# Kernel tuning notes

Hardware: AMD Instinct MI355X
Metric: run time of the kernel (lower is better)

The kernel has to match this reference:

```python
import jax, jax.numpy as jnp
import numpy as np

NUM_EXPERTS = 64
HIDDEN = 2048
SINKHORN_ITERS = 30
EPS = 1e-08


def setup_inputs() -> dict:
    key = jax.random.key(0)
    k1, k2 = jax.random.split(key)
    hidden_states = jax.random.normal(k1, (4, 2048, HIDDEN), dtype=jnp.float32)
    # torch Linear default init ~ U(-1/sqrt(H), 1/sqrt(H))
    bound = 1.0 / np.sqrt(HIDDEN)
    W = jax.random.uniform(k2, (NUM_EXPERTS, HIDDEN), dtype=jnp.float32,
                           minval=-bound, maxval=bound)
    return {"hidden_states": hidden_states, "W": W}


def _sinkhorn(cost, num_iters=SINKHORN_ITERS):
    # cost: (T, E) float32 logits
    cost = jnp.exp(cost)
    T, E = cost.shape
    d0 = jnp.ones((T,), dtype=cost.dtype)
    d1 = jnp.ones((E,), dtype=cost.dtype)

    def body(i, carry):
        d0, d1 = carry
        d0 = (1.0 / T) / (jnp.sum(d1 * cost, axis=1) + EPS)
        d1 = (1.0 / E) / (jnp.sum(d0[:, None] * cost, axis=0) + EPS)
        return (d0, d1)

    d0, d1 = jax.lax.fori_loop(0, num_iters, body, (d0, d1))
    return d1 * cost * d0[:, None]


def reference(hidden_states, W):
    # router logits: (B, S, H) @ (H, E) -> flatten to (T, E)
    logits = jnp.einsum('bsh,eh->bse', hidden_states, W)
    router_logits = logits.reshape(-1, NUM_EXPERTS)
    # expert affinities (original uses float64 sigmoid; use float32 for jax default)
    expert_affinities = jax.nn.sigmoid(router_logits.astype(jnp.float32))
    expert_affinities = expert_affinities.astype(hidden_states.dtype)
    # Sinkhorn balancing on detached logits (training path)
    sinkroute = _sinkhorn(jax.lax.stop_gradient(router_logits).astype(jnp.float32))
    expert_index = jnp.argmax(sinkroute, axis=1, keepdims=True).astype(jnp.int32)
    return (router_logits, expert_affinities, expert_index)
```

## Files before the change

kernel.cpp:

```cpp
#include <hip/hip_runtime.h>
#include <math.h>

#define T_TOKENS 8192
#define NEXP 64
#define HID 2048
#define NITER 30
#define SINK_BLOCKS 32
#define KSEG 4
#define WREG 131072

typedef __bf16 bf16_t;
typedef bf16_t bf16x8 __attribute__((ext_vector_type(8)));
typedef float  f32x4  __attribute__((ext_vector_type(4)));

__device__ __forceinline__ void gload_lds16(const void* g, void* l) {
    __builtin_amdgcn_global_load_lds(
        (const __attribute__((address_space(1))) unsigned int*)g,
        (__attribute__((address_space(3))) unsigned int*)l, 16, 0, 0);
}

__global__ __launch_bounds__(256)
void prep_whl(const float* __restrict__ W, bf16_t* __restrict__ wsw)
{
    int gid = blockIdx.x * 256 + threadIdx.x;
    int region = gid >> 14;
    int qid = gid & 16383;
    int c = qid >> 9, L = qid & 511;
    int r = L >> 3, slot = L & 7;
    int qi = slot ^ (r & 7);
    const float* src = W + (size_t)r * HID + c * 64 + qi * 8;
    float4 v0 = *(const float4*)src;
    float4 v1 = *(const float4*)(src + 4);
    float x[8] = {v0.x, v0.y, v0.z, v0.w, v1.x, v1.y, v1.z, v1.w};
    bf16x8 q;
#pragma unroll
    for (int i = 0; i < 8; i++) {
        bf16_t h = (bf16_t)x[i];
        q[i] = (region == 0) ? h : (bf16_t)(x[i] - (float)h);
    }
    *(bf16x8*)(wsw + (size_t)region * WREG + (size_t)qid * 8) = q;
}

__global__ __launch_bounds__(256, 3)
void gemm_splitk(const float* __restrict__ A, const bf16_t* __restrict__ Wq,
                 float* __restrict__ part)
{
    __shared__ float  sA[2][32 * 64];
    __shared__ bf16_t sW[2][2][64 * 64];

    const int tid = threadIdx.x, lane = tid & 63, wv = tid >> 6;
    const int ks   = blockIdx.x & 3;
    const int tok0 = (blockIdx.x >> 2) * 32;
    const int mgrp = wv >> 1, ngrp = wv & 1;
    const int g = lane >> 4, m = lane & 15;
    const int arow = mgrp * 16 + m;
    const int m7 = m & 7;

    f32x4 acc0 = {0.f, 0.f, 0.f, 0.f}, acc1 = {0.f, 0.f, 0.f, 0.f};

    int ap[2], acs[2];
#pragma unroll
    for (int j = 0; j < 2; j++) {
        int p = (wv * 2 + j) * 64 + lane;
        ap[j] = p;
        int r = p >> 4, slot = p & 15;
        acs[j] = slot ^ (r & 7);
    }

#define STAGE_CHUNK(cc, dst)                                                    \
    {                                                                           \
        const int _cc = (cc);                                                   \
        _Pragma("unroll")                                                       \
        for (int j = 0; j < 2; j++) {                                           \
            int r = ap[j] >> 4;                                                 \
            const float* src = A + (size_t)(tok0 + r) * HID + ks * 512          \
                             + _cc * 64 + acs[j] * 4;                           \
            gload_lds16(src, &sA[dst][(wv * 2 + j) * 256]);                     \
        }                                                                       \
        const size_t chb = ((size_t)(ks * 8 + _cc) * 512) * 8;                  \
        _Pragma("unroll")                                                       \
        for (int j = 0; j < 2; j++) {                                           \
            size_t q8 = chb + (size_t)((wv * 2 + j) * 64 + lane) * 8;           \
            gload_lds16(Wq + q8,        &sW[dst][0][(wv * 2 + j) * 512]);       \
            gload_lds16(Wq + WREG + q8, &sW[dst][1][(wv * 2 + j) * 512]);       \
        }                                                                       \
    }

    STAGE_CHUNK(0, 0);
    __syncthreads();

    for (int cc = 0; cc < 8; ++cc) {
        const int buf = cc & 1, nb = buf ^ 1;
        if (cc + 1 < 8) STAGE_CHUNK(cc + 1, nb);

        const float*  sAc = sA[buf];
        const bf16_t* sWh = sW[buf][0];
        const bf16_t* sWl = sW[buf][1];
#pragma unroll
        for (int k32 = 0; k32 < 2; ++k32) {
            int s0 = (k32 * 8 + g * 2) ^ m7;
            float4 x0 = *(const float4*)&sAc[arow * 64 + s0 * 4];
            float4 x1 = *(const float4*)&sAc[arow * 64 + (s0 ^ 1) * 4];
            float xs[8] = {x0.x, x0.y, x0.z, x0.w, x1.x, x1.y, x1.z, x1.w};
            bf16x8 fAh, fAl;
#pragma unroll
            for (int i = 0; i < 8; i++) {
                bf16_t h = (bf16_t)xs[i];
                fAh[i] = h; fAl[i] = (bf16_t)(xs[i] - (float)h);
            }
            const int q = k32 * 4 + g;
            {
                int off = (ngrp * 32 + m) * 64 + (q ^ m7) * 8;
                bf16x8 fWh = *(const bf16x8*)&sWh[off];
                bf16x8 fWl = *(const bf16x8*)&sWl[off];
                acc0 = __builtin_amdgcn_mfma_f32_16x16x32_bf16(fAh, fWh, acc0, 0, 0, 0);
                acc0 = __builtin_amdgcn_mfma_f32_16x16x32_bf16(fAh, fWl, acc0, 0, 0, 0);
                acc0 = __builtin_amdgcn_mfma_f32_16x16x32_bf16(fAl, fWh, acc0, 0, 0, 0);
            }
            {
                int off = (ngrp * 32 + 16 + m) * 64 + (q ^ m7) * 8;
                bf16x8 fWh = *(const bf16x8*)&sWh[off];
                bf16x8 fWl = *(const bf16x8*)&sWl[off];
                acc1 = __builtin_amdgcn_mfma_f32_16x16x32_bf16(fAh, fWh, acc1, 0, 0, 0);
                acc1 = __builtin_amdgcn_mfma_f32_16x16x32_bf16(fAh, fWl, acc1, 0, 0, 0);
                acc1 = __builtin_amdgcn_mfma_f32_16x16x32_bf16(fAl, fWh, acc1, 0, 0, 0);
            }
        }
        __syncthreads();
    }

    float* pb = part + (size_t)ks * T_TOKENS * 64;
#pragma unroll
    for (int i = 0; i < 4; i++) {
        int t = tok0 + mgrp * 16 + g * 4 + i;
        pb[(size_t)t * 64 + ngrp * 32 + m]      = acc0[i];
        pb[(size_t)t * 64 + ngrp * 32 + 16 + m] = acc1[i];
    }
#undef STAGE_CHUNK
}

__global__ __launch_bounds__(256, 1)
void sinkhorn_v5(const float* __restrict__ part,
                 float* __restrict__ out,
                 float* __restrict__ sd)
{
    __shared__ float tileT[64][260];
    __shared__ float d0_lds[256];
    __shared__ float d1_lds[64];
    __shared__ float pl[4][64];
    const int tid = threadIdx.x, bid = blockIdx.x;
    const int t = bid * 256 + tid;

    float* logits = out;
    float* aff    = out + (size_t)T_TOKENS * 64;
    float* idx    = out + (size_t)2 * T_TOKENS * 64;

    float c[64];
#pragma unroll
    for (int e4 = 0; e4 < 16; e4++) {
        float4 v = *(const float4*)(part + (size_t)t * 64 + e4 * 4);
#pragma unroll
        for (int s = 1; s < KSEG; s++) {
            float4 p = *(const float4*)(part + (size_t)s * T_TOKENS * 64
                                             + (size_t)t * 64 + e4 * 4);
            v.x += p.x; v.y += p.y; v.z += p.z; v.w += p.w;
        }
        *(float4*)(logits + (size_t)t * 64 + e4 * 4) = v;
        float4 sg;
        sg.x = (v.x >= 0.f) ? 1.f / (1.f + expf(-v.x)) : expf(v.x) / (1.f + expf(v.x));
        sg.y = (v.y >= 0.f) ? 1.f / (1.f + expf(-v.y)) : expf(v.y) / (1.f + expf(v.y));
        sg.z = (v.z >= 0.f) ? 1.f / (1.f + expf(-v.z)) : expf(v.z) / (1.f + expf(v.z));
        sg.w = (v.w >= 0.f) ? 1.f / (1.f + expf(-v.w)) : expf(v.w) / (1.f + expf(v.w));
        *(float4*)(aff + (size_t)t * 64 + e4 * 4) = sg;
        c[e4 * 4 + 0] = expf(v.x);
        c[e4 * 4 + 1] = expf(v.y);
        c[e4 * 4 + 2] = expf(v.z);
        c[e4 * 4 + 3] = expf(v.w);
    }
#pragma unroll
    for (int e = 0; e < 64; e++) tileT[e][tid] = c[e];
    if (tid < 64) d1_lds[tid] = 1.0f;
    __syncthreads();

    const int pe = tid & 63, pq = tid >> 6;
    float d0 = 0.f;

    for (int iter = 0; iter < NITER; ++iter) {
        float s = 0.f;
#pragma unroll
        for (int e4 = 0; e4 < 16; e4++) {
            float4 dv = *(const float4*)(&d1_lds[e4 * 4]);
            s = fmaf(c[e4 * 4 + 0], dv.x, s);
            s = fmaf(c[e4 * 4 + 1], dv.y, s);
            s = fmaf(c[e4 * 4 + 2], dv.z, s);
            s = fmaf(c[e4 * 4 + 3], dv.w, s);
        }
        d0 = (1.0f / 8192.0f) / (s + 1e-8f);
        d0_lds[tid] = d0;
        __syncthreads();

        float cs = 0.f;
        const float* rowp = &tileT[pe][pq * 64];
        const float* d0p  = &d0_lds[pq * 64];
#pragma unroll
        for (int j = 0; j < 16; j++) {
            float4 cv = *(const float4*)(rowp + j * 4);
            float4 dv = *(const float4*)(d0p + j * 4);
            cs = fmaf(cv.x, dv.x, cs);
            cs = fmaf(cv.y, dv.y, cs);
            cs = fmaf(cv.z, dv.z, cs);
            cs = fmaf(cv.w, dv.w, cs);
        }
        pl[pq][pe] = cs;
        __syncthreads();

        if (tid < 64) {
            float S = pl[0][tid] + pl[1][tid] + pl[2][tid] + pl[3][tid];
            __hip_atomic_store(&sd[(size_t)(iter * SINK_BLOCKS + bid) * 64 + tid], S,
                               __ATOMIC_RELAXED, __HIP_MEMORY_SCOPE_AGENT);
            const float* base = sd + (size_t)iter * SINK_BLOCKS * 64 + tid;
            float v[SINK_BLOCKS];
            bool ok = false; int guard = 0;
            while (!ok && guard++ < (1 << 20)) {
                ok = true;
#pragma unroll
                for (int b = 0; b < SINK_BLOCKS; b++)
                    v[b] = __hip_atomic_load(base + b * 64, __ATOMIC_RELAXED,
                                             __HIP_MEMORY_SCOPE_AGENT);
#pragma unroll
                for (int b = 0; b < SINK_BLOCKS; b++) ok = ok && (v[b] > 0.f);
            }
            float S2 = 0.f;
#pragma unroll
            for (int b = 0; b < SINK_BLOCKS; b++) S2 += v[b];
            d1_lds[tid] = (1.0f / 64.0f) / (S2 + 1e-8f);
        }
        __syncthreads();
    }

    float best = -1.0f; int bi = 0;
#pragma unroll
    for (int e4 = 0; e4 < 16; e4++) {
        float4 dv = *(const float4*)(&d1_lds[e4 * 4]);
        float vv0 = (dv.x * c[e4 * 4 + 0]) * d0;
        float vv1 = (dv.y * c[e4 * 4 + 1]) * d0;
        float vv2 = (dv.z * c[e4 * 4 + 2]) * d0;
        float vv3 = (dv.w * c[e4 * 4 + 3]) * d0;
        if (vv0 > best) { best = vv0; bi = e4 * 4 + 0; }
        if (vv1 > best) { best = vv1; bi = e4 * 4 + 1; }
        if (vv2 > best) { best = vv2; bi = e4 * 4 + 2; }
        if (vv3 > best) { best = vv3; bi = e4 * 4 + 3; }
    }
    idx[t] = (float)bi;
}

extern "C" void kernel_launch(void* const* d_in, const int* in_sizes, int n_in,
                              void* d_out, int out_size, void* d_ws, size_t ws_size,
                              hipStream_t stream)
{
    (void)in_sizes; (void)n_in; (void)out_size; (void)ws_size;
    const float* hs = (const float*)d_in[0];
    const float* W  = (const float*)d_in[1];
    float* out      = (float*)d_out;

    bf16_t* wsw  = (bf16_t*)d_ws;
    float*  part = (float*)d_ws + 131072;
    float*  sd   = part + (size_t)KSEG * T_TOKENS * 64;

    prep_whl<<<128, 256, 0, stream>>>(W, wsw);
    gemm_splitk<<<1024, 256, 0, stream>>>(hs, wsw, part);
    sinkhorn_v5<<<SINK_BLOCKS, 256, 0, stream>>>(part, out, sd);
}
```

Baseline: 237.1 us.

## Halve split-K segments and use two-level hierarchical cross-block Sinkhorn reduction

The GEMM now splits K into 2 segments instead of 4, which halves the partial-sum writes and reads, launches 512 blocks with double the chunk loop, and lowers the occupancy hint from 3 to 2. The Sinkhorn kernel replaces the flat all-to-all polling of 32 block partials with a two-level tree: 8 blocks each combine 4 partials into a second buffer, and every block then polls only 8 values. The LDS tile row stride also changes from 260 to 261. The aim is to cut spin-polling traffic per iteration and partial-sum memory traffic, at the cost of an extra dependent hop in each iteration and less GEMM parallelism.

```diff
diff --git a/kernel.cpp b/kernel.cpp
--- a/kernel.cpp
+++ b/kernel.cpp
@@ -6,7 +6,6 @@
 #define HID 2048
 #define NITER 30
 #define SINK_BLOCKS 32
-#define KSEG 4
 #define WREG 131072
 
 typedef __bf16 bf16_t;
@@ -41,7 +40,7 @@
     *(bf16x8*)(wsw + (size_t)region * WREG + (size_t)qid * 8) = q;
 }
 
-__global__ __launch_bounds__(256, 3)
+__global__ __launch_bounds__(256, 2)
 void gemm_splitk(const float* __restrict__ A, const bf16_t* __restrict__ Wq,
                  float* __restrict__ part)
 {
@@ -49,8 +48,8 @@
     __shared__ bf16_t sW[2][2][64 * 64];
 
     const int tid = threadIdx.x, lane = tid & 63, wv = tid >> 6;
-    const int ks   = blockIdx.x & 3;
-    const int tok0 = (blockIdx.x >> 2) * 32;
+    const int ks   = blockIdx.x & 1;
+    const int tok0 = (blockIdx.x >> 1) * 32;
     const int mgrp = wv >> 1, ngrp = wv & 1;
     const int g = lane >> 4, m = lane & 15;
     const int arow = mgrp * 16 + m;
@@ -73,11 +72,11 @@
         _Pragma("unroll")                                                       \
         for (int j = 0; j < 2; j++) {                                           \
             int r = ap[j] >> 4;                                                 \
-            const float* src = A + (size_t)(tok0 + r) * HID + ks * 512          \
+            const float* src = A + (size_t)(tok0 + r) * HID + ks * 1024         \
                              + _cc * 64 + acs[j] * 4;                           \
             gload_lds16(src, &sA[dst][(wv * 2 + j) * 256]);                     \
         }                                                                       \
-        const size_t chb = ((size_t)(ks * 8 + _cc) * 512) * 8;                  \
+        const size_t chb = ((size_t)(ks * 16 + _cc) * 512) * 8;                 \
         _Pragma("unroll")                                                       \
         for (int j = 0; j < 2; j++) {                                           \
             size_t q8 = chb + (size_t)((wv * 2 + j) * 64 + lane) * 8;           \
@@ -89,9 +88,9 @@
     STAGE_CHUNK(0, 0);
     __syncthreads();
 
-    for (int cc = 0; cc < 8; ++cc) {
+    for (int cc = 0; cc < 16; ++cc) {
         const int buf = cc & 1, nb = buf ^ 1;
-        if (cc + 1 < 8) STAGE_CHUNK(cc + 1, nb);
+        if (cc + 1 < 16) STAGE_CHUNK(cc + 1, nb);
 
         const float*  sAc = sA[buf];
         const bf16_t* sWh = sW[buf][0];
@@ -140,11 +139,12 @@
 }
 
 __global__ __launch_bounds__(256, 1)
-void sinkhorn_v5(const float* __restrict__ part,
+void sinkhorn_v6(const float* __restrict__ part,
                  float* __restrict__ out,
-                 float* __restrict__ sd)
-{
-    __shared__ float tileT[64][260];
+                 float* __restrict__ sd1,
+                 float* __restrict__ sd2)
+{
+    __shared__ float tileT[64][261];
     __shared__ float d0_lds[256];
     __shared__ float d1_lds[64];
     __shared__ float pl[4][64];
@@ -155,16 +155,15 @@
     float* aff    = out + (size_t)T_TOKENS * 64;
     float* idx    = out + (size_t)2 * T_TOKENS * 64;
 
+    const float* p0 = part + (size_t)t * 64;
+    const float* p1 = part + (size_t)T_TOKENS * 64 + (size_t)t * 64;
+
     float c[64];
 #pragma unroll
     for (int e4 = 0; e4 < 16; e4++) {
-        float4 v = *(const float4*)(part + (size_t)t * 64 + e4 * 4);
-#pragma unroll
-        for (int s = 1; s < KSEG; s++) {
-            float4 p = *(const float4*)(part + (size_t)s * T_TOKENS * 64
-                                             + (size_t)t * 64 + e4 * 4);
-            v.x += p.x; v.y += p.y; v.z += p.z; v.w += p.w;
-        }
+        float4 a = *(const float4*)(p0 + e4 * 4);
+        float4 b = *(const float4*)(p1 + e4 * 4);
+        float4 v = {a.x + b.x, a.y + b.y, a.z + b.z, a.w + b.w};
         *(float4*)(logits + (size_t)t * 64 + e4 * 4) = v;
         float4 sg;
         sg.x = (v.x >= 0.f) ? 1.f / (1.f + expf(-v.x)) : expf(v.x) / (1.f + expf(v.x));
@@ -216,23 +215,36 @@
 
         if (tid < 64) {
             float S = pl[0][tid] + pl[1][tid] + pl[2][tid] + pl[3][tid];
-            __hip_atomic_store(&sd[(size_t)(iter * SINK_BLOCKS + bid) * 64 + tid], S,
+            __hip_atomic_store(&sd1[(size_t)(iter * SINK_BLOCKS + bid) * 64 + tid], S,
                                __ATOMIC_RELAXED, __HIP_MEMORY_SCOPE_AGENT);
-            const float* base = sd + (size_t)iter * SINK_BLOCKS * 64 + tid;
-            float v[SINK_BLOCKS];
-            bool ok = false; int guard = 0;
-            while (!ok && guard++ < (1 << 20)) {
-                ok = true;
-#pragma unroll
-                for (int b = 0; b < SINK_BLOCKS; b++)
-                    v[b] = __hip_atomic_load(base + b * 64, __ATOMIC_RELAXED,
+            if (bid < 8) {
+                const float* b0 = sd1 + ((size_t)iter * SINK_BLOCKS + bid * 4) * 64 + tid;
+                float v[4]; bool ok = false; int gg = 0;
+                while (!ok && gg++ < (1 << 20)) {
+                    ok = true;
+#pragma unroll
+                    for (int j = 0; j < 4; j++)
+                        v[j] = __hip_atomic_load(b0 + j * 64, __ATOMIC_RELAXED,
+                                                 __HIP_MEMORY_SCOPE_AGENT);
+#pragma unroll
+                    for (int j = 0; j < 4; j++) ok = ok && (v[j] > 0.f);
+                }
+                float L = (v[0] + v[1]) + (v[2] + v[3]);
+                __hip_atomic_store(&sd2[(size_t)(iter * 8 + bid) * 64 + tid], L,
+                                   __ATOMIC_RELAXED, __HIP_MEMORY_SCOPE_AGENT);
+            }
+            const float* c0 = sd2 + (size_t)iter * 8 * 64 + tid;
+            float w[8]; bool ok2 = false; int g2 = 0;
+            while (!ok2 && g2++ < (1 << 20)) {
+                ok2 = true;
+#pragma unroll
+                for (int j = 0; j < 8; j++)
+                    w[j] = __hip_atomic_load(c0 + j * 64, __ATOMIC_RELAXED,
                                              __HIP_MEMORY_SCOPE_AGENT);
 #pragma unroll
-                for (int b = 0; b < SINK_BLOCKS; b++) ok = ok && (v[b] > 0.f);
-            }
-            float S2 = 0.f;
-#pragma unroll
-            for (int b = 0; b < SINK_BLOCKS; b++) S2 += v[b];
+                for (int j = 0; j < 8; j++) ok2 = ok2 && (w[j] > 0.f);
+            }
+            float S2 = ((w[0] + w[1]) + (w[2] + w[3])) + ((w[4] + w[5]) + (w[6] + w[7]));
             d1_lds[tid] = (1.0f / 64.0f) / (S2 + 1e-8f);
         }
         __syncthreads();
@@ -265,9 +277,10 @@
 
     bf16_t* wsw  = (bf16_t*)d_ws;
     float*  part = (float*)d_ws + 131072;
-    float*  sd   = part + (size_t)KSEG * T_TOKENS * 64;
+    float*  sd1  = part + (size_t)2 * T_TOKENS * 64;
+    float*  sd2  = sd1 + NITER * SINK_BLOCKS * 64;
 
     prep_whl<<<128, 256, 0, stream>>>(W, wsw);
-    gemm_splitk<<<1024, 256, 0, stream>>>(hs, wsw, part);
-    sinkhorn_v5<<<SINK_BLOCKS, 256, 0, stream>>>(part, out, sd);
-}
+    gemm_splitk<<<512, 256, 0, stream>>>(hs, wsw, part);
+    sinkhorn_v6<<<SINK_BLOCKS, 256, 0, stream>>>(part, out, sd1, sd2);
+}
```

After: 235.7 us. About the same (-0.6%).
